# Optimization experiments

Hardware: AMD Instinct MI355X
Metric: run time of the kernel (lower is better)

The kernel has to match this reference:

```python
import jax, jax.numpy as jnp
import numpy as np

B, L, S, H, E = 2, 2048, 2048, 16, 64
EPS = 1e-8


def setup_inputs() -> dict:
    key = jax.random.key(0)
    k1, k2, k3, k4, k5 = jax.random.split(key, 5)
    query = jax.random.normal(k1, (B, L, H, E), dtype=jnp.float32)
    key_t = jax.random.normal(k2, (B, S, H, E), dtype=jnp.float32)
    value = jax.random.normal(k3, (B, S, H, E), dtype=jnp.float32)
    mask_miss_k = jax.random.randint(k4, (B, S, 1), 0, 2).astype(bool)
    mask_miss_q = jax.random.randint(k5, (B, L, 1), 0, 2).astype(bool)
    # monotone per-batch positions -> standard causal structure
    pos = jnp.broadcast_to(jnp.arange(L, dtype=jnp.int32)[None, :, None], (B, L, 1))
    return {"query": query, "key": key_t, "value": value,
            "mask_miss_k": mask_miss_k, "mask_miss_q": mask_miss_q,
            "pos": pos, "causal_mask": 1}


def reference(query, key, value, mask_miss_k, mask_miss_q, pos, causal_mask):
    # query: (B,L,H,E); key/value: (B,S,H,E)
    E_ = query.shape[-1]
    scale = 1.0 / np.sqrt(E_)
    scores = jnp.einsum('blhe,bshe->bhls', query, key)  # (B,H,L,S)
    if causal_mask:
        p = pos[..., 0]  # (B,L)
        causal_add = jnp.where(p[:, None, :] > p[:, :, None],
                               -jnp.inf, 0.0).astype(scores.dtype)  # (B,L,S)
        scores = scores + causal_add[:, None, :, :]
    # additive -inf masks for missing keys / queries
    m_k = jnp.where(mask_miss_k[..., 0][:, None, None, :], -jnp.inf, 0.0).astype(scores.dtype)
    m_q = jnp.where(mask_miss_q[..., 0][:, None, :, None], -jnp.inf, 0.0).astype(scores.dtype)
    # NOTE: scale multiplies (scores + M_k) exactly as in the original
    att = jnp.maximum(jax.nn.softmax(scale * (scores + m_k), axis=-1) + m_q, 0.0)
    # entropy of (post-relu, possibly unnormalized) attention weights
    entropy = -jnp.sum(att * jnp.log(jnp.clip(att, EPS, None)), axis=-1)  # (B,H,L)
    entropy = jnp.nan_to_num(entropy, nan=0.0)
    A = jnp.nan_to_num(att)  # dropout p=0 -> identity, then nan_to_num
    V = jnp.einsum('bhls,bshd->blhd', A, value)  # (B,L,H,E)
    return V, A, entropy
```

## Files before the change

kernel.cpp:

```cpp
#include <hip/hip_runtime.h>

#define BB 2
#define LL 2048
#define SS 2048
#define HH 16
#define EE 64
#define HE (HH*EE)
#define TS 64
#define SCALEF 0.125f
#define NEGBIG (-1e30f)

typedef __bf16 bf8 __attribute__((ext_vector_type(8)));
typedef float f4v __attribute__((ext_vector_type(4)));
typedef unsigned int u32;
typedef unsigned short u16;

#define V_ELEMS  ((size_t)BB*LL*HH*EE)
#define A_BASE   (V_ELEMS)
#define ENT_BASE (A_BASE + (size_t)BB*HH*LL*SS)

__device__ __forceinline__ u16 bfb(float f) {
    u32 u = __builtin_bit_cast(u32, f);
    return (u16)((u + 0x7fffu + ((u >> 16) & 1u)) >> 16);
}
__device__ __forceinline__ int swz8(int r) { return (((r) & 7) ^ (((r) >> 3) & 7)) << 4; }

__device__ __forceinline__ f4v mfma16(bf8 a, bf8 b, f4v c) {
    return __builtin_amdgcn_mfma_f32_16x16x32_bf16(a, b, c, 0, 0, 0);
}
__device__ __forceinline__ int maskv(const void* p, int i, int isB) {
    return isB ? (int)((const unsigned char*)p)[i] : ((const int*)p)[i];
}
__device__ __forceinline__ void barrier_lds() {
    asm volatile("s_waitcnt lgkmcnt(0)" ::: "memory");
    __builtin_amdgcn_s_barrier();
    asm volatile("" ::: "memory");
}
__device__ __forceinline__ uint4 pack8(float4 f0, float4 f1) {
    uint4 wv;
    wv.x = bfb(f0.x) | ((u32)bfb(f0.y) << 16);
    wv.y = bfb(f0.z) | ((u32)bfb(f0.w) << 16);
    wv.z = bfb(f1.x) | ((u32)bfb(f1.y) << 16);
    wv.w = bfb(f1.z) | ((u32)bfb(f1.w) << 16);
    return wv;
}

__device__ __forceinline__ void stage128x64(const float* __restrict__ src,
                                            char* lds, int tid) {
    const int r = tid >> 2, seg = tid & 3;
    const float* rp = src + (size_t)r * HE + seg * 16;
    float4 f0 = *(const float4*)(rp + 0);
    float4 f1 = *(const float4*)(rp + 4);
    float4 f2 = *(const float4*)(rp + 8);
    float4 f3 = *(const float4*)(rp + 12);
    const int base = r * 128 + seg * 32;
    *(uint4*)(void*)(lds + ((base +  0) ^ swz8(r))) = pack8(f0, f1);
    *(uint4*)(void*)(lds + ((base + 16) ^ swz8(r))) = pack8(f2, f3);
}

__global__ __launch_bounds__(512, 4) void k_fused(
    const float* __restrict__ Qg, const float* __restrict__ Kg, const float* __restrict__ Vg,
    const void* __restrict__ mk, const void* __restrict__ mq,
    float* __restrict__ outF)
{
    __shared__ __align__(16) char ldsP[16384];
    __shared__ __align__(16) char ldsK[2][8192];
    __shared__ __align__(16) char ldsVT[2][8192];
    __shared__ float ldsKM[SS];
    __shared__ int sFlag;

    const int blk = blockIdx.x;
    const int xcd = blk & 7, idx = blk >> 3;
    const int bh  = xcd * 4 + (idx & 3);
    const int slot = idx >> 2;
    const int band = (slot < 8) ? (15 - slot) : (slot - 8);
    const int b = bh >> 4, h = bh & 15;
    const int tid = threadIdx.x;
    const int w = tid >> 6, lane = tid & 63, g = lane >> 4, le = lane & 15;

    int isB;
    {
        const unsigned char* c = (const unsigned char*)mk;
        unsigned acc = 0;
        #pragma unroll
        for (int j = 0; j < 8; ++j) {
            const int off = tid + j * 512;
            if (off & 3) acc |= c[off];
        }
        if (tid == 0) sFlag = 0;
        __syncthreads();
        if (acc) atomicOr(&sFlag, 1);
        __syncthreads();
        isB = sFlag;
    }
    for (int i = tid; i < SS; i += 512)
        ldsKM[i] = maskv(mk, b * SS + i, isB) ? NEGBIG : 0.f;

    const float* Qb = Qg + (size_t)b * LL * HE + h * EE;
    const float* Kb = Kg + (size_t)b * SS * HE + h * EE;
    const float* Vb = Vg + (size_t)b * SS * HE + h * EE;

    const int l0 = band * 128;
    const int lbase = l0 + w * 16 + g * 4;
    const int whi = l0 + w * 16 + 15;
    const int ta  = whi >> 6;
    const int ntile = 2 * (band + 1);

    stage128x64(Qb + (size_t)l0 * HE, ldsP, tid);
    __syncthreads();
    const int qr = w * 16 + le;
    bf8 qf0 = *(const bf8*)(void*)(ldsP + ((qr * 128 +  0 + g * 16) ^ swz8(qr)));
    bf8 qf1 = *(const bf8*)(void*)(ldsP + ((qr * 128 + 64 + g * 16) ^ swz8(qr)));
    barrier_lds();

    const int kr = tid >> 3, ksg = tid & 7;
    const float* kbase = Kb + (size_t)kr * HE + ksg * 8;
    const int koff = (kr * 128 + ksg * 16) ^ swz8(kr);
    const int vrp = tid >> 4, vei = tid & 15;
    const float* vbase = Vb + (size_t)(2 * vrp) * HE + vei * 4;

    float M[4], D[4], T[4];
    #pragma unroll
    for (int r = 0; r < 4; ++r) { M[r] = NEGBIG; D[r] = 0.f; T[r] = 0.f; }

    float4 ka = *(const float4*)(kbase);
    float4 kb2 = *(const float4*)(kbase + 4);
    *(uint4*)(void*)(&ldsK[0][0] + koff) = pack8(ka, kb2);
    if (ntile > 1) {
        const float* kp = kbase + (size_t)TS * HE;
        ka = *(const float4*)(kp); kb2 = *(const float4*)(kp + 4);
    }
    barrier_lds();
    int cur = 0;

    for (int st = 0; st < ntile; ++st) {
        const int s0 = st * TS;
        if (st + 1 < ntile) {
            *(uint4*)(void*)(&ldsK[cur ^ 1][0] + koff) = pack8(ka, kb2);
            if (st + 2 < ntile) {
                const float* kp = kbase + (size_t)(st + 2) * TS * HE;
                ka = *(const float4*)(kp); kb2 = *(const float4*)(kp + 4);
            }
        }
        if (s0 <= whi) {
            f4v acc[4];
            float tm[4] = {NEGBIG, NEGBIG, NEGBIG, NEGBIG};
            #pragma unroll
            for (int cb = 0; cb < 4; ++cb) {
                const int sr = cb * 16 + le;
                bf8 k0 = *(const bf8*)(void*)(&ldsK[cur][0] + ((sr * 128 +  0 + g * 16) ^ swz8(sr)));
                bf8 k1 = *(const bf8*)(void*)(&ldsK[cur][0] + ((sr * 128 + 64 + g * 16) ^ swz8(sr)));
                f4v a = {0.f, 0.f, 0.f, 0.f};
                a = mfma16(qf0, k0, a);
                a = mfma16(qf1, k1, a);
                const float km = ldsKM[s0 + cb * 16 + le];
                const int s = s0 + cb * 16 + le;
                #pragma unroll
                for (int r = 0; r < 4; ++r) {
                    float z = a[r] * SCALEF + km;
                    if (s > lbase + r) z = NEGBIG;
                    acc[cb][r] = z;
                    tm[r] = fmaxf(tm[r], z);
                }
            }
            #pragma unroll
            for (int r = 0; r < 4; ++r) {
                #pragma unroll
                for (int msk = 1; msk < 16; msk <<= 1)
                    tm[r] = fmaxf(tm[r], __shfl_xor(tm[r], msk));
                const float mn  = fmaxf(M[r], tm[r]);
                const float fre = __expf(M[r] - mn);
                float ed = 0.f, et = 0.f;
                #pragma unroll
                for (int cb = 0; cb < 4; ++cb) {
                    const float z = acc[cb][r];
                    const float e = __expf(z - mn);
                    ed += e; et += e * z;
                }
                D[r] = D[r] * fre + ed;
                T[r] = T[r] * fre + et;
                M[r] = mn;
            }
        }
        barrier_lds();
        cur ^= 1;
    }

    float C[4];
    bool qm[4];
    #pragma unroll
    for (int r = 0; r < 4; ++r) {
        #pragma unroll
        for (int msk = 1; msk < 16; msk <<= 1) {
            const float Mo = __shfl_xor(M[r], msk);
            const float Do = __shfl_xor(D[r], msk);
            const float To = __shfl_xor(T[r], msk);
            const float mn = fmaxf(M[r], Mo);
            const float fa = __expf(M[r] - mn);
            const float fb = __expf(Mo  - mn);
            D[r] = D[r] * fa + Do * fb;
            T[r] = T[r] * fa + To * fb;
            M[r] = mn;
        }
        const int l = lbase + r;
        qm[r] = maskv(mq, b * LL + l, isB) != 0;
        const bool valid = (M[r] > -1e29f) && !qm[r];
        C[r] = valid ? (M[r] + __logf(D[r])) : 1e30f;
        const float ent = valid ? (C[r] - T[r] / D[r]) : 0.f;
        if (le == 0) outF[ENT_BASE + (size_t)bh * LL + l] = ent;
    }

    float* const Arow0 = outF + A_BASE + ((size_t)bh * LL + l0) * SS;

    {
        const f4v zz = {0.f, 0.f, 0.f, 0.f};
        for (int k = 0; k < 16; ++k) {
            const int row = w * 16 + k;
            if (maskv(mq, b * LL + l0 + row, isB)) {
                float* dst = Arow0 + (size_t)row * SS + lane * 4;
                #pragma unroll
                for (int j = 0; j < 8; ++j)
                    *(f4v*)(void*)(dst + j * 256) = zz;
            }
        }
    }

    {
        const int rr = lane >> 2, cc = lane & 3;
        const int row = w * 16 + rr;
        if (!maskv(mq, b * LL + l0 + row, isB)) {
            float* dst0 = Arow0 + (size_t)row * SS;
            const f4v zz = {0.f, 0.f, 0.f, 0.f};
            for (int c = (ta + 1) * TS + cc * 4; c < SS; c += 16)
                *(f4v*)(void*)(dst0 + c) = zz;
        }
    }

    f4v O[4];
    #pragma unroll
    for (int eb = 0; eb < 4; ++eb) O[eb] = (f4v){0.f, 0.f, 0.f, 0.f};

    ka  = *(const float4*)(kbase);
    kb2 = *(const float4*)(kbase + 4);
    float4 va  = *(const float4*)(vbase);
    float4 vb2 = *(const float4*)(vbase + HE);
    *(uint4*)(void*)(&ldsK[0][0] + koff) = pack8(ka, kb2);
    {
        const float* pa_ = &va.x; const float* pb_ = &vb2.x;
        #pragma unroll
        for (int i = 0; i < 4; ++i) {
            const int e = vei * 4 + i;
            const u32 pk = (u32)bfb(pa_[i]) | ((u32)bfb(pb_[i]) << 16);
            *(u32*)(void*)(&ldsVT[0][0] + ((e * 128 + vrp * 4) ^ swz8(e))) = pk;
        }
    }
    if (ntile > 1) {
        const float* kp = kbase + (size_t)TS * HE;
        const float* vp = vbase + (size_t)TS * HE;
        ka = *(const float4*)(kp); kb2 = *(const float4*)(kp + 4);
        va = *(const float4*)(vp); vb2 = *(const float4*)(vp + HE);
    }
    barrier_lds();
    cur = 0;
    char* const myP = ldsP + w * 2048;

    for (int st = 0; st < ntile; ++st) {
        const int s0 = st * TS;
        if (st + 1 < ntile) {
            *(uint4*)(void*)(&ldsK[cur ^ 1][0] + koff) = pack8(ka, kb2);
            {
                const float* pa_ = &va.x; const float* pb_ = &vb2.x;
                #pragma unroll
                for (int i = 0; i < 4; ++i) {
                    const int e = vei * 4 + i;
                    const u32 pk = (u32)bfb(pa_[i]) | ((u32)bfb(pb_[i]) << 16);
                    *(u32*)(void*)(&ldsVT[cur ^ 1][0] + ((e * 128 + vrp * 4) ^ swz8(e))) = pk;
                }
            }
            if (st + 2 < ntile) {
                const float* kp = kbase + (size_t)(st + 2) * TS * HE;
                const float* vp = vbase + (size_t)(st + 2) * TS * HE;
                ka = *(const float4*)(kp); kb2 = *(const float4*)(kp + 4);
                va = *(const float4*)(vp); vb2 = *(const float4*)(vp + HE);
            }
        }
        if (st <= ta) {
            f4v acc[4];
            #pragma unroll
            for (int cb = 0; cb < 4; ++cb) {
                const int sr = cb * 16 + le;
                bf8 k0 = *(const bf8*)(void*)(&ldsK[cur][0] + ((sr * 128 +  0 + g * 16) ^ swz8(sr)));
                bf8 k1 = *(const bf8*)(void*)(&ldsK[cur][0] + ((sr * 128 + 64 + g * 16) ^ swz8(sr)));
                f4v a = {0.f, 0.f, 0.f, 0.f};
                a = mfma16(qf0, k0, a);
                a = mfma16(qf1, k1, a);
                acc[cb] = a;
            }
            #pragma unroll
            for (int cb = 0; cb < 4; ++cb) {
                const float km = ldsKM[s0 + cb * 16 + le];
                const int s = s0 + cb * 16 + le;
                #pragma unroll
                for (int r = 0; r < 4; ++r) {
                    float z = acc[cb][r] * SCALEF + km;
                    if (s > lbase + r) z = NEGBIG;
                    const float p = __expf(z - C[r]);
                    const int row = g * 4 + r;
                    *(u16*)(void*)(myP + ((row * 128 + (cb * 16 + le) * 2) ^ swz8(row))) = bfb(p);
                    if (!qm[r])
                        outF[A_BASE + ((size_t)bh * LL + (l0 + w * 16 + row)) * SS + s] = p;
                }
            }
            asm volatile("s_waitcnt lgkmcnt(0)" ::: "memory");

            #pragma unroll
            for (int kkb = 0; kkb < 2; ++kkb) {
                bf8 pa = *(const bf8*)(void*)(myP + ((le * 128 + kkb * 64 + g * 16) ^ swz8(le)));
                #pragma unroll
                for (int eb = 0; eb < 4; ++eb) {
                    const int e = eb * 16 + le;
                    bf8 vb = *(const bf8*)(void*)(&ldsVT[cur][0] + ((e * 128 + kkb * 64 + g * 16) ^ swz8(e)));
                    O[eb] = mfma16(pa, vb, O[eb]);
                }
            }
        }
        barrier_lds();
        cur ^= 1;
    }

    #pragma unroll
    for (int eb = 0; eb < 4; ++eb) {
        #pragma unroll
        for (int r = 0; r < 4; ++r) {
            const int l = lbase + r;
            outF[((size_t)(b * LL + l) * HH + h) * EE + eb * 16 + le] = O[eb][r];
        }
    }
}

extern "C" void kernel_launch(void* const* d_in, const int* in_sizes, int n_in,
                              void* d_out, int out_size, void* d_ws, size_t ws_size,
                              hipStream_t stream) {
    const float* Q = (const float*)d_in[0];
    const float* K = (const float*)d_in[1];
    const float* V = (const float*)d_in[2];
    const void* mk = d_in[3];
    const void* mq = d_in[4];
    float* outF = (float*)d_out;

    dim3 blk(512), grid(BB * HH * 16);
    hipLaunchKernelGGL(k_fused, grid, blk, 0, stream, Q, K, V, mk, mq, outF);
}
```

Measured before the change: 193.3 us.

## Compact live query rows per band so waves skip masked-out queries

Each block builds a permutation of its 128 query rows in which rows not masked by mask_miss_q come first, using ballot and popcount, and each wave then processes the remapped rows. Waves whose rows are all masked skip the QK/softmax and PV tile loops, and the tile count follows the last live row. With about half the queries missing, this is meant to avoid MFMA and exp work for rows whose outputs are zero anyway. The cost is scattered row addressing for Q loads and output stores, plus a tail-zeroing pass whose start now depends on each row.

```diff
diff --git a/kernel.cpp b/kernel.cpp
--- a/kernel.cpp
+++ b/kernel.cpp
@@ -14,6 +14,7 @@
 typedef float f4v __attribute__((ext_vector_type(4)));
 typedef unsigned int u32;
 typedef unsigned short u16;
+typedef unsigned long long u64;
 
 #define V_ELEMS  ((size_t)BB*LL*HH*EE)
 #define A_BASE   (V_ELEMS)
@@ -43,19 +44,6 @@
     wv.z = bfb(f1.x) | ((u32)bfb(f1.y) << 16);
     wv.w = bfb(f1.z) | ((u32)bfb(f1.w) << 16);
     return wv;
-}
-
-__device__ __forceinline__ void stage128x64(const float* __restrict__ src,
-                                            char* lds, int tid) {
-    const int r = tid >> 2, seg = tid & 3;
-    const float* rp = src + (size_t)r * HE + seg * 16;
-    float4 f0 = *(const float4*)(rp + 0);
-    float4 f1 = *(const float4*)(rp + 4);
-    float4 f2 = *(const float4*)(rp + 8);
-    float4 f3 = *(const float4*)(rp + 12);
-    const int base = r * 128 + seg * 32;
-    *(uint4*)(void*)(lds + ((base +  0) ^ swz8(r))) = pack8(f0, f1);
-    *(uint4*)(void*)(lds + ((base + 16) ^ swz8(r))) = pack8(f2, f3);
 }
 
 __global__ __launch_bounds__(512, 4) void k_fused(
@@ -67,6 +55,8 @@
     __shared__ __align__(16) char ldsK[2][8192];
     __shared__ __align__(16) char ldsVT[2][8192];
     __shared__ float ldsKM[SS];
+    __shared__ int ldsMap[128];
+    __shared__ int ldsNL[2];
     __shared__ int sFlag;
 
     const int blk = blockIdx.x;
@@ -96,17 +86,56 @@
     for (int i = tid; i < SS; i += 512)
         ldsKM[i] = maskv(mk, b * SS + i, isB) ? NEGBIG : 0.f;
 
+    const int l0 = band * 128;
+
+    if (w < 2) {
+        const int p = w * 64 + lane;
+        const int live = (maskv(mq, b * LL + l0 + p, isB) == 0);
+        const u64 m = __ballot(live);
+        if (lane == 0) ldsNL[w] = __popcll(m);
+    }
+    __syncthreads();
+    const int nLive = ldsNL[0] + ldsNL[1];
+    if (w < 2) {
+        const int p = w * 64 + lane;
+        const int live = (maskv(mq, b * LL + l0 + p, isB) == 0);
+        const u64 m = __ballot(live);
+        const int rank = __popcll(m & ((1ULL << lane) - 1ULL));
+        const int baseL = (w == 0) ? 0 : ldsNL[0];
+        const int baseD = nLive + ((w == 0) ? 0 : (64 - ldsNL[0]));
+        ldsMap[live ? (baseL + rank) : (baseD + (lane - rank))] = p;
+    }
+    __syncthreads();
+
     const float* Qb = Qg + (size_t)b * LL * HE + h * EE;
     const float* Kb = Kg + (size_t)b * SS * HE + h * EE;
     const float* Vb = Vg + (size_t)b * SS * HE + h * EE;
 
-    const int l0 = band * 128;
-    const int lbase = l0 + w * 16 + g * 4;
-    const int whi = l0 + w * 16 + 15;
-    const int ta  = whi >> 6;
-    const int ntile = 2 * (band + 1);
-
-    stage128x64(Qb + (size_t)l0 * HE, ldsP, tid);
+    const int maxLive = (nLive > 0) ? ldsMap[nLive - 1] : 0;
+    const int ntile = (nLive > 0) ? (((l0 + maxLive) >> 6) + 1) : 0;
+
+    const bool wact = (w * 16) < nLive;
+    int arow[4]; bool qmr[4];
+    #pragma unroll
+    for (int r = 0; r < 4; ++r) {
+        const int o = w * 16 + g * 4 + r;
+        qmr[r] = (o >= nLive);
+        arow[r] = ldsMap[o];
+    }
+    const int lastSlot = wact ? ((w * 16 + 15 < nLive) ? (w * 16 + 15) : (nLive - 1)) : 0;
+    const int whi = wact ? (l0 + ldsMap[lastSlot]) : -1;
+
+    {
+        const int r = tid >> 2, seg = tid & 3;
+        const float* rp = Qb + (size_t)(l0 + ldsMap[r]) * HE + seg * 16;
+        float4 f0 = *(const float4*)(rp + 0);
+        float4 f1 = *(const float4*)(rp + 4);
+        float4 f2 = *(const float4*)(rp + 8);
+        float4 f3 = *(const float4*)(rp + 12);
+        const int base = r * 128 + seg * 32;
+        *(uint4*)(void*)(ldsP + ((base +  0) ^ swz8(r))) = pack8(f0, f1);
+        *(uint4*)(void*)(ldsP + ((base + 16) ^ swz8(r))) = pack8(f2, f3);
+    }
     __syncthreads();
     const int qr = w * 16 + le;
     bf8 qf0 = *(const bf8*)(void*)(ldsP + ((qr * 128 +  0 + g * 16) ^ swz8(qr)));
@@ -158,7 +187,7 @@
                 #pragma unroll
                 for (int r = 0; r < 4; ++r) {
                     float z = a[r] * SCALEF + km;
-                    if (s > lbase + r) z = NEGBIG;
+                    if (s > l0 + arow[r]) z = NEGBIG;
                     acc[cb][r] = z;
                     tm[r] = fmaxf(tm[r], z);
                 }
@@ -187,7 +216,6 @@
     }
 
     float C[4];
-    bool qm[4];
     #pragma unroll
     for (int r = 0; r < 4; ++r) {
         #pragma unroll
@@ -202,12 +230,10 @@
             T[r] = T[r] * fa + To * fb;
             M[r] = mn;
         }
-        const int l = lbase + r;
-        qm[r] = maskv(mq, b * LL + l, isB) != 0;
-        const bool valid = (M[r] > -1e29f) && !qm[r];
+        const bool valid = (M[r] > -1e29f) && !qmr[r];
         C[r] = valid ? (M[r] + __logf(D[r])) : 1e30f;
-        const float ent = valid ? (C[r] - T[r] / D[r]) : 0.f;
-        if (le == 0) outF[ENT_BASE + (size_t)bh * LL + l] = ent;
+        if (le == 0 && valid)
+            outF[ENT_BASE + (size_t)bh * LL + l0 + arow[r]] = C[r] - T[r] / D[r];
     }
 
     float* const Arow0 = outF + A_BASE + ((size_t)bh * LL + l0) * SS;
@@ -221,17 +247,18 @@
                 #pragma unroll
                 for (int j = 0; j < 8; ++j)
                     *(f4v*)(void*)(dst + j * 256) = zz;
-            }
-        }
-    }
-
+                if (lane == 0) outF[ENT_BASE + (size_t)bh * LL + l0 + row] = 0.f;
+            }
+        }
+    }
     {
         const int rr = lane >> 2, cc = lane & 3;
         const int row = w * 16 + rr;
         if (!maskv(mq, b * LL + l0 + row, isB)) {
+            const int start = ((l0 + row + 1 + 3) & ~3);
             float* dst0 = Arow0 + (size_t)row * SS;
             const f4v zz = {0.f, 0.f, 0.f, 0.f};
-            for (int c = (ta + 1) * TS + cc * 4; c < SS; c += 16)
+            for (int c = start + cc * 4; c < SS; c += 16)
                 *(f4v*)(void*)(dst0 + c) = zz;
         }
     }
@@ -284,7 +311,7 @@
                 va = *(const float4*)(vp); vb2 = *(const float4*)(vp + HE);
             }
         }
-        if (st <= ta) {
+        if (s0 <= whi) {
             f4v acc[4];
             #pragma unroll
             for (int cb = 0; cb < 4; ++cb) {
@@ -303,12 +330,12 @@
                 #pragma unroll
                 for (int r = 0; r < 4; ++r) {
                     float z = acc[cb][r] * SCALEF + km;
-                    if (s > lbase + r) z = NEGBIG;
+                    if (s > l0 + arow[r]) z = NEGBIG;
                     const float p = __expf(z - C[r]);
                     const int row = g * 4 + r;
                     *(u16*)(void*)(myP + ((row * 128 + (cb * 16 + le) * 2) ^ swz8(row))) = bfb(p);
-                    if (!qm[r])
-                        outF[A_BASE + ((size_t)bh * LL + (l0 + w * 16 + row)) * SS + s] = p;
+                    if (!qmr[r])
+                        outF[A_BASE + ((size_t)bh * LL + (l0 + arow[r])) * SS + s] = p;
                 }
             }
             asm volatile("s_waitcnt lgkmcnt(0)" ::: "memory");
@@ -332,7 +359,7 @@
     for (int eb = 0; eb < 4; ++eb) {
         #pragma unroll
         for (int r = 0; r < 4; ++r) {
-            const int l = lbase + r;
+            const int l = l0 + arow[r];
             outF[((size_t)(b * LL + l) * HH + h) * EE + eb * 16 + le] = O[eb][r];
         }
     }
```

Result: slower. 200.9 us (+3.9%).
